# Optimization experiments

Hardware: AMD Instinct MI355X
Metric: run time of the kernel (lower is better)

## Reference

```python
import jax, jax.numpy as jnp
import numpy as np

DIM = 512
NUM_HEADS = 8
HEAD_DIM = DIM // NUM_HEADS
SOFT_CAP = 50.0
EPS = 1e-6
ROPE_BASE = 10000.0


def _rope_cos_sin(T):
    inv_freq = 1.0 / (ROPE_BASE ** (jnp.arange(0, HEAD_DIM, 2, dtype=jnp.float32) / HEAD_DIM))
    t = jnp.arange(T, dtype=jnp.float32)
    freqs = jnp.einsum('t,f->tf', t, inv_freq)            # (T, HEAD_DIM//2)
    emb = jnp.concatenate([freqs, freqs], axis=-1)         # (T, HEAD_DIM)
    return jnp.cos(emb), jnp.sin(emb)


def _rotate_half(x):
    x1, x2 = jnp.split(x, 2, axis=-1)
    return jnp.concatenate([-x2, x1], axis=-1)


def _apply_rope(x, cos, sin):
    # x: (B,H,T,hd); cos/sin: (T,hd) broadcast over B,H
    return x * cos + _rotate_half(x) * sin


def _rmsnorm(x, g):
    var = jnp.mean(jnp.square(x), axis=-1, keepdims=True)
    return x * jax.lax.rsqrt(var + EPS) * g


def setup_inputs() -> dict:
    key = jax.random.key(0)
    ks = jax.random.split(key, 7)
    B, T = 256, 256
    s = 1.0 / np.sqrt(DIM)
    return {
        'x': jax.random.normal(ks[0], (B, T, DIM), dtype=jnp.float32),
        'wq': jax.random.normal(ks[1], (DIM, DIM), dtype=jnp.float32) * s,
        'wk': jax.random.normal(ks[2], (DIM, DIM), dtype=jnp.float32) * s,
        'wv': jax.random.normal(ks[3], (DIM, DIM), dtype=jnp.float32) * s,
        'wo': jax.random.normal(ks[4], (DIM, DIM), dtype=jnp.float32) * s,
        'gq': jnp.ones((HEAD_DIM,), dtype=jnp.float32),
        'gk': jnp.ones((HEAD_DIM,), dtype=jnp.float32),
    }


def reference(x, wq, wk, wv, wo, gq, gk):
    B, T, D = x.shape
    H, hd = NUM_HEADS, HEAD_DIM
    scale = hd ** -0.5

    def proj(w):
        return jnp.einsum('btd,ed->bte', x, w).reshape(B, T, H, hd).transpose(0, 2, 1, 3)

    q = proj(wq)  # (B,H,T,hd)
    k = proj(wk)
    v = proj(wv)

    q = _rmsnorm(q, gq)
    k = _rmsnorm(k, gk)

    cos, sin = _rope_cos_sin(T)
    q = _apply_rope(q, cos, sin)
    k = _apply_rope(k, cos, sin)

    attn = jnp.einsum('bhqd,bhkd->bhqk', q, k) * scale
    attn = SOFT_CAP * jnp.tanh(attn / SOFT_CAP)
    causal = jnp.tril(jnp.ones((T, T), dtype=bool))
    attn = jnp.where(causal, attn, -jnp.inf)
    attn = jax.nn.softmax(attn.astype(jnp.float32), axis=-1).astype(v.dtype)

    out = jnp.einsum('bhqk,bhkd->bhqd', attn, v)
    out = out.transpose(0, 2, 1, 3).reshape(B, T, D)
    return jnp.einsum('btd,ed->bte', out, wo)
```

## Files before the change

### kernel.cpp

```cpp
#include <hip/hip_runtime.h>
#include <cstdint>
#include <cstddef>

#define B_   256
#define T_   256
#define D_   512
#define H_   8
#define HD_  64
#define BT_  65536
#define KDIM 512

typedef __bf16 bf16x8_t __attribute__((ext_vector_type(8)));
typedef __bf16 bf16x4_t __attribute__((ext_vector_type(4)));
typedef float  f32x4_t  __attribute__((ext_vector_type(4)));

__device__ __forceinline__ void gload16(const void* gp, void* lp) {
  __builtin_amdgcn_global_load_lds(
      (const __attribute__((address_space(1))) void*)gp,
      (__attribute__((address_space(3))) void*)lp, 16, 0, 0);
}

#define BAR()   __builtin_amdgcn_s_barrier()
#define SCB()   __builtin_amdgcn_sched_barrier(0)
#define LGKM0() asm volatile("s_waitcnt lgkmcnt(0)" ::: "memory")

__global__ __launch_bounds__(256) void prep(
    const float* __restrict__ x,
    const float* __restrict__ wq, const float* __restrict__ wk,
    const float* __restrict__ wv, const float* __restrict__ wo,
    __bf16* __restrict__ xb, __bf16* __restrict__ wb,
    float* __restrict__ rc, float* __restrict__ rs) {
  const int b = blockIdx.x;
  if (b < 2048) {
    for (size_t i = (size_t)b * 256 + threadIdx.x; i < 8388608UL; i += 524288UL) {
      f32x4_t v = *(const f32x4_t*)&x[i * 4];
      bf16x4_t o;
      o[0] = (__bf16)v[0]; o[1] = (__bf16)v[1]; o[2] = (__bf16)v[2]; o[3] = (__bf16)v[3];
      *(bf16x4_t*)&xb[i * 4] = o;
    }
  } else if (b < 2304) {
    for (int i = (b - 2048) * 256 + threadIdx.x; i < 262144; i += 65536) {
      int which = i >> 16;
      int off   = (i & 65535) * 4;
      const float* src = (which == 0) ? wq : (which == 1) ? wk : (which == 2) ? wv : wo;
      f32x4_t v = *(const f32x4_t*)&src[off];
      bf16x4_t o;
      o[0] = (__bf16)v[0]; o[1] = (__bf16)v[1]; o[2] = (__bf16)v[2]; o[3] = (__bf16)v[3];
      *(bf16x4_t*)&wb[(size_t)which * 262144 + off] = o;
    }
  } else {
    int idx = (b - 2304) * 256 + threadIdx.x;
    if (idx < T_ * 32) {
      int t = idx >> 5, j = idx & 31;
      float inv = powf(10000.f, -(float)j * (1.0f / 32.0f));
      float a = (float)t * inv;
      rc[idx] = cosf(a);
      rs[idx] = sinf(a);
    }
  }
}

template <int MODE>
__global__ __launch_bounds__(512, 2) void gemm256(
    const __bf16* __restrict__ A, const __bf16* __restrict__ W,
    void* __restrict__ outp) {
  __shared__ __bf16 lds[65536];
  const int tid = threadIdx.x;
  const int lane = tid & 63, w = tid >> 6;
  const int wm = w >> 2, wn = w & 3;
  const int l15 = lane & 15, lg = lane >> 4;
  const int swl = l15 & 7;

  const int cpx = gridDim.x >> 3;
  const int swz = (blockIdx.x & 7) * cpx + (blockIdx.x >> 3);
  const int bz = swz >> 9;
  const int by = (swz >> 1) & 255;
  const int bx = swz & 1;
  const int m0 = by * 256, n0 = bx * 256;

  const __bf16* Ag = A + (size_t)m0 * KDIM;
  const __bf16* Bg = W + (size_t)bz * (KDIM * KDIM) + (size_t)n0 * KDIM;
  const int srow = tid >> 3;
  const int scol = (((tid & 7) ^ ((tid >> 3) & 7)) * 8);

#define STAGE(J) do {                                                        \
    const int T__ = (J) >> 2, r__ = (J) & 3;                                 \
    const int h__ = r__ >> 1;                                                \
    const int isB__ = (r__ == 1 || r__ == 2);                                \
    const size_t grow__ = (size_t)(h__ * 128 + srow) * KDIM + T__ * 64 + scol; \
    const __bf16* gp__ = isB__ ? (Bg + grow__) : (Ag + grow__);              \
    __bf16* lp__ = &lds[(T__ & 1) * 32768 + isB__ * 16384 + (h__ * 128 + w * 8) * 64]; \
    gload16(gp__, lp__);                                                     \
    gload16(gp__ + 64 * KDIM, lp__ + 64 * 64);                               \
  } while (0)

  f32x4_t acc[8][4];
#pragma unroll
  for (int i = 0; i < 8; i++)
#pragma unroll
    for (int j = 0; j < 4; j++) acc[i][j] = (f32x4_t){0.f, 0.f, 0.f, 0.f};

  bf16x8_t a0[4][2], a1[4][2], b0[2][2], b1[2][2];

#define PH_A(P, STJ) do {                                                    \
    const int ab__ = (P) * 32768;                                            \
    _Pragma("unroll") for (int i = 0; i < 4; i++)                            \
      _Pragma("unroll") for (int s = 0; s < 2; s++)                          \
        a0[i][s] = *(const bf16x8_t*)&lds[ab__ + (wm * 64 + i * 16 + l15) * 64 + (((s * 4 + lg) ^ swl) << 3)]; \
    _Pragma("unroll") for (int j = 0; j < 2; j++)                            \
      _Pragma("unroll") for (int s = 0; s < 2; s++)                          \
        b0[j][s] = *(const bf16x8_t*)&lds[ab__ + 16384 + (wn * 32 + j * 16 + l15) * 64 + (((s * 4 + lg) ^ swl) << 3)]; \
    if ((STJ) >= 0) STAGE(STJ);                                              \
    SCB(); BAR(); LGKM0(); SCB();                                            \
    __builtin_amdgcn_s_setprio(1);                                           \
    _Pragma("unroll") for (int i = 0; i < 4; i++)                            \
      _Pragma("unroll") for (int j = 0; j < 2; j++) {                        \
        acc[i][j] = __builtin_amdgcn_mfma_f32_16x16x32_bf16(a0[i][0], b0[j][0], acc[i][j], 0, 0, 0); \
        acc[i][j] = __builtin_amdgcn_mfma_f32_16x16x32_bf16(a0[i][1], b0[j][1], acc[i][j], 0, 0, 0); \
      }                                                                      \
    __builtin_amdgcn_s_setprio(0); SCB(); BAR();                             \
  } while (0)

#define PH_B(P, STJ) do {                                                    \
    const int ab__ = (P) * 32768;                                            \
    _Pragma("unroll") for (int j = 0; j < 2; j++)                            \
      _Pragma("unroll") for (int s = 0; s < 2; s++)                          \
        b1[j][s] = *(const bf16x8_t*)&lds[ab__ + 16384 + (128 + wn * 32 + j * 16 + l15) * 64 + (((s * 4 + lg) ^ swl) << 3)]; \
    if ((STJ) >= 0) STAGE(STJ);                                              \
    SCB(); BAR(); LGKM0(); SCB();                                            \
    __builtin_amdgcn_s_setprio(1);                                           \
    _Pragma("unroll") for (int i = 0; i < 4; i++)                            \
      _Pragma("unroll") for (int j = 0; j < 2; j++) {                        \
        acc[i][j + 2] = __builtin_amdgcn_mfma_f32_16x16x32_bf16(a0[i][0], b1[j][0], acc[i][j + 2], 0, 0, 0); \
        acc[i][j + 2] = __builtin_amdgcn_mfma_f32_16x16x32_bf16(a0[i][1], b1[j][1], acc[i][j + 2], 0, 0, 0); \
      }                                                                      \
    __builtin_amdgcn_s_setprio(0); SCB(); BAR();                             \
  } while (0)

#define PH_C(P, STJ) do {                                                    \
    const int ab__ = (P) * 32768;                                            \
    _Pragma("unroll") for (int i = 0; i < 4; i++)                            \
      _Pragma("unroll") for (int s = 0; s < 2; s++)                          \
        a1[i][s] = *(const bf16x8_t*)&lds[ab__ + (128 + wm * 64 + i * 16 + l15) * 64 + (((s * 4 + lg) ^ swl) << 3)]; \
    if ((STJ) >= 0) STAGE(STJ);                                              \
    SCB(); BAR(); LGKM0(); SCB();                                            \
    __builtin_amdgcn_s_setprio(1);                                           \
    _Pragma("unroll") for (int i = 0; i < 4; i++)                            \
      _Pragma("unroll") for (int j = 0; j < 2; j++) {                        \
        acc[i + 4][j + 2] = __builtin_amdgcn_mfma_f32_16x16x32_bf16(a1[i][0], b1[j][0], acc[i + 4][j + 2], 0, 0, 0); \
        acc[i + 4][j + 2] = __builtin_amdgcn_mfma_f32_16x16x32_bf16(a1[i][1], b1[j][1], acc[i + 4][j + 2], 0, 0, 0); \
      }                                                                      \
    __builtin_amdgcn_s_setprio(0); SCB(); BAR();                             \
  } while (0)

#define PH_D(P, STJ, VM) do {                                                \
    if ((STJ) >= 0) STAGE(STJ);                                              \
    SCB(); BAR();                                                            \
    __builtin_amdgcn_s_setprio(1);                                           \
    _Pragma("unroll") for (int i = 0; i < 4; i++)                            \
      _Pragma("unroll") for (int j = 0; j < 2; j++) {                        \
        acc[i + 4][j] = __builtin_amdgcn_mfma_f32_16x16x32_bf16(a1[i][0], b0[j][0], acc[i + 4][j], 0, 0, 0); \
        acc[i + 4][j] = __builtin_amdgcn_mfma_f32_16x16x32_bf16(a1[i][1], b0[j][1], acc[i + 4][j], 0, 0, 0); \
      }                                                                      \
    __builtin_amdgcn_s_setprio(0);                                           \
    if ((VM) == 6) asm volatile("s_waitcnt vmcnt(6)" ::: "memory");          \
    else if ((VM) == 0) asm volatile("s_waitcnt vmcnt(0)" ::: "memory");     \
    SCB(); BAR();                                                            \
  } while (0)

  STAGE(0); STAGE(1); STAGE(2); STAGE(3); STAGE(4); STAGE(5); STAGE(6);
  asm volatile("s_waitcnt vmcnt(6)" ::: "memory");
  SCB(); BAR();

#pragma unroll 1
  for (int tp = 0; tp < 3; ++tp) {
    const int g0 = tp * 8;
    PH_A(0, g0 + 7);  PH_B(0, g0 + 8);  PH_C(0, g0 + 9);  PH_D(0, g0 + 10, 6);
    PH_A(1, g0 + 11); PH_B(1, g0 + 12); PH_C(1, g0 + 13); PH_D(1, g0 + 14, 6);
  }
  PH_A(0, 31); PH_B(0, -1); PH_C(0, -1); PH_D(0, -1, 0);
  PH_A(1, -1); PH_B(1, -1); PH_C(1, -1); PH_D(1, -1, -1);

#undef PH_A
#undef PH_B
#undef PH_C
#undef PH_D
#undef STAGE

#pragma unroll
  for (int i = 0; i < 8; i++) {
#pragma unroll
    for (int rr = 0; rr < 4; rr++) {
      const int m = m0 + (i >> 2) * 128 + wm * 64 + (i & 3) * 16 + lg * 4 + rr;
      if (MODE == 0) {
        __bf16* outz = (__bf16*)outp + (size_t)bz * ((size_t)BT_ * D_);
        const int bb = m >> 8, tt = m & 255;
        const size_t rbase = ((size_t)bb * H_) * T_ * HD_ + (size_t)tt * HD_;
#pragma unroll
        for (int j = 0; j < 4; j++) {
          const int c = n0 + (j >> 1) * 128 + wn * 32 + (j & 1) * 16 + l15;
          const int hh = c >> 6, dd = c & 63;
          outz[rbase + (size_t)hh * (T_ * HD_) + dd] = (__bf16)acc[i][j][rr];
        }
      } else {
        float* outf = (float*)outp;
#pragma unroll
        for (int j = 0; j < 4; j++) {
          const int c = n0 + (j >> 1) * 128 + wn * 32 + (j & 1) * 16 + l15;
          outf[(size_t)m * D_ + c] = acc[i][j][rr];
        }
      }
    }
  }
}

__global__ __launch_bounds__(256) void norm_rope(
    __bf16* __restrict__ qb, __bf16* __restrict__ kb,
    const float* __restrict__ gq, const float* __restrict__ gk,
    const float* __restrict__ rc, const float* __restrict__ rs) {
  const int gid = blockIdx.x * 256 + threadIdx.x;
  const int wid = gid >> 6;
  const int lane = gid & 63;
  const int l2 = lane & 31;
  const int half = lane >> 5;
  const int nw = (gridDim.x * 256) >> 6;
  const int NROWS = B_ * H_ * T_;
  for (int idx = wid; idx < NROWS; idx += nw) {
    int ri = idx * 2 + half;
    int isk = ri >= NROWS;
    int r = isk ? ri - NROWS : ri;
    __bf16* base = isk ? kb : qb;
    const float* g = isk ? gk : gq;
    size_t off = (size_t)r * HD_ + 2 * l2;
    unsigned u = *(const unsigned*)&base[off];
    float v0 = (float)__builtin_bit_cast(__bf16, (unsigned short)(u & 0xffffu));
    float v1 = (float)__builtin_bit_cast(__bf16, (unsigned short)(u >> 16));
    float ss = v0 * v0 + v1 * v1;
#pragma unroll
    for (int m = 1; m < 32; m <<= 1) ss += __shfl_xor(ss, m);
    float rn = rsqrtf(ss * (1.0f / HD_) + 1e-6f);
    v0 *= rn * g[2 * l2];
    v1 *= rn * g[2 * l2 + 1];
    int t = r & (T_ - 1);
    int j0 = (2 * l2) & 31;
    float c0 = rc[t * 32 + j0], c1 = rc[t * 32 + j0 + 1];
    float s0 = rs[t * 32 + j0], s1 = rs[t * 32 + j0 + 1];
    float p0 = __shfl_xor(v0, 16);
    float p1 = __shfl_xor(v1, 16);
    float sg = (l2 < 16) ? -1.f : 1.f;
    float o0 = v0 * c0 + sg * p0 * s0;
    float o1 = v1 * c1 + sg * p1 * s1;
    unsigned short h0 = __builtin_bit_cast(unsigned short, (__bf16)o0);
    unsigned short h1 = __builtin_bit_cast(unsigned short, (__bf16)o1);
    *(unsigned*)&base[off] = (unsigned)h0 | ((unsigned)h1 << 16);
  }
}

__global__ __launch_bounds__(512, 2) void attn_kernel(
    const __bf16* __restrict__ qb, const __bf16* __restrict__ kb,
    const __bf16* __restrict__ vb, __bf16* __restrict__ ob) {
  __shared__ __bf16 Kl[256 * 64];
  __shared__ __bf16 VT[64 * 256];
  __shared__ __bf16 Pl[8 * 16 * 64];
  const int bh = blockIdx.x;
  const __bf16* Qg = qb + (size_t)bh * (T_ * HD_);
  const __bf16* Kg = kb + (size_t)bh * (T_ * HD_);
  const __bf16* Vg = vb + (size_t)bh * (T_ * HD_);
  const int tid = threadIdx.x, lane = tid & 63, w = tid >> 6;
  const int bI = bh >> 3, hI = bh & 7;

#pragma unroll
  for (int p = 0; p < 4; p++) {
    const int t = p * 64 + (tid >> 3);
    const int a = tid & 7;
    const int d0 = a * 8;
    *(bf16x8_t*)&Kl[t * 64 + (((a ^ (t & 7)) << 3))] =
        *(const bf16x8_t*)&Kg[t * HD_ + d0];
    bf16x8_t vv = *(const bf16x8_t*)&Vg[t * HD_ + d0];
#pragma unroll
    for (int j = 0; j < 8; j++) {
      const int row = d0 + j;
      const int rk = (row & 7) ^ ((row >> 3) & 7);
      VT[row * 256 + (((t >> 3) ^ rk) << 3) + (t & 7)] = vv[j];
    }
  }
  __syncthreads();

  const int l15 = lane & 15;
  const int lg = lane >> 4;
  const int sw = l15 & 7;
  const f32x4_t zero = {0.f, 0.f, 0.f, 0.f};
  const float C1 = 0.0072134752f;
  const float LOG2E = 1.44269504f;

  for (int half = 0; half < 2; half++) {
    const int qt = half ? (15 - w) : w;
    const int q0 = qt * 16;
    bf16x8_t aq0 = *(const bf16x8_t*)&Qg[(q0 + l15) * HD_ + lg * 8];
    bf16x8_t aq1 = *(const bf16x8_t*)&Qg[(q0 + l15) * HD_ + 32 + lg * 8];
    const int ntiles_e = (qt + 2) & ~1;
    const int qr = q0 + (lg << 2);

    f32x4_t ls = {0.f, 0.f, 0.f, 0.f};
    f32x4_t o[4];
#pragma unroll
    for (int j = 0; j < 4; j++) o[j] = zero;

    for (int t0 = 0; t0 < ntiles_e; t0 += 4) {
      const int te = (t0 + 4 < ntiles_e) ? (t0 + 4) : ntiles_e;
      for (int n = t0; n < te; ++n) {
        bf16x8_t kb0 = *(const bf16x8_t*)&Kl[(n * 16 + l15) * 64 + ((lg ^ sw) << 3)];
        bf16x8_t kb1 = *(const bf16x8_t*)&Kl[(n * 16 + l15) * 64 + (((4 + lg) ^ sw) << 3)];
        f32x4_t a = __builtin_amdgcn_mfma_f32_16x16x32_bf16(aq0, kb0, zero, 0, 0, 0);
        a = __builtin_amdgcn_mfma_f32_16x16x32_bf16(aq1, kb1, a, 0, 0, 0);
        const int key = n * 16 + l15;
        const int lsl = ((n - t0) << 1) + (l15 >> 3);
#pragma unroll
        for (int r = 0; r < 4; r++) {
          float e2 = __builtin_amdgcn_exp2f(a[r] * C1);
          float cm = -100.f * __builtin_amdgcn_rcpf(e2 + 1.f);
          float p = __builtin_amdgcn_exp2f(cm * LOG2E);
          p = (key <= qr + r) ? p : 0.f;
          ls[r] += p;
          const int ro = (lg << 2) + r;
          Pl[w * 1024 + ro * 64 + ((lsl ^ (ro & 7)) << 3) + (l15 & 7)] = (__bf16)p;
        }
      }
      asm volatile("s_waitcnt lgkmcnt(0)" ::: "memory");
      __builtin_amdgcn_sched_barrier(0);
      const int nkc = (te - t0) >> 1;
      for (int kcc = 0; kcc < nkc; ++kcc) {
        bf16x8_t pa = *(const bf16x8_t*)&Pl[w * 1024 + l15 * 64 + (((kcc * 4 + lg) ^ sw) << 3)];
#pragma unroll
        for (int j = 0; j < 4; j++) {
          const int row = j * 16 + l15;
          const int rk = sw ^ ((2 * j + (l15 >> 3)) & 7);
          const int sl = (t0 << 1) + kcc * 4 + lg;
          bf16x8_t bv = *(const bf16x8_t*)&VT[row * 256 + ((sl ^ rk) << 3)];
          o[j] = __builtin_amdgcn_mfma_f32_16x16x32_bf16(pa, bv, o[j], 0, 0, 0);
        }
      }
    }

#pragma unroll
    for (int off = 1; off < 16; off <<= 1) {
#pragma unroll
      for (int r = 0; r < 4; r++) ls[r] += __shfl_xor(ls[r], off);
    }

    float rl[4];
#pragma unroll
    for (int r = 0; r < 4; r++) rl[r] = 1.0f / ls[r];
#pragma unroll
    for (int j = 0; j < 4; j++) {
      int dd = j * 16 + l15;
#pragma unroll
      for (int r = 0; r < 4; r++) {
        int q = qr + r;
        ob[((size_t)(bI * T_ + q)) * D_ + hI * HD_ + dd] = (__bf16)(o[j][r] * rl[r]);
      }
    }
  }
}

extern "C" void kernel_launch(void* const* d_in, const int* in_sizes, int n_in,
                              void* d_out, int out_size, void* d_ws, size_t ws_size,
                              hipStream_t stream) {
  (void)in_sizes; (void)n_in; (void)out_size; (void)ws_size;
  const float* x  = (const float*)d_in[0];
  const float* wq = (const float*)d_in[1];
  const float* wk = (const float*)d_in[2];
  const float* wv = (const float*)d_in[3];
  const float* wo = (const float*)d_in[4];
  const float* gq = (const float*)d_in[5];
  const float* gk = (const float*)d_in[6];

  char* ws = (char*)d_ws;
  __bf16* xb   = (__bf16*)ws;
  __bf16* qkvb = (__bf16*)(ws + 67108864UL);
  __bf16* qb = qkvb;
  __bf16* kb = qkvb + 33554432UL;
  __bf16* vb = qkvb + 67108864UL;
  __bf16* wb = (__bf16*)(ws + 4UL * 67108864UL);
  float*  rc = (float*)(ws + 4UL * 67108864UL + 2097152UL);
  float*  rs = rc + 8192;
  __bf16* ob = xb;

  prep<<<dim3(2336), 256, 0, stream>>>(x, wq, wk, wv, wo, xb, wb, rc, rs);
  gemm256<0><<<dim3(1536), 512, 0, stream>>>(xb, wb, (void*)qkvb);
  norm_rope<<<dim3(2048), 256, 0, stream>>>(qb, kb, gq, gk, rc, rs);
  attn_kernel<<<dim3(2048), 512, 0, stream>>>(qb, kb, vb, ob);
  gemm256<1><<<dim3(512), 512, 0, stream>>>(ob, wb + 3UL * 262144UL, d_out);
}
```

Before: 356.7 us.

## Make GEMM blocks loop over all N tiles for one M tile

Both GEMM launches now give each block one 256-row M tile and loop over every output N tile in turn (six jobs for QKV, two for the output projection). The load pipeline keeps prefetching across job boundaries, and each job is stored before the accumulators are cleared. The grid drops from 1536/512 blocks to 256. The aim is to remove per-block prologue and drain cost and keep the A tile hot in cache, at the cost of only one block per CU, which gives less latency hiding than the 2-per-CU launch bounds allow.

```diff
diff --git a/kernel.cpp b/kernel.cpp
--- a/kernel.cpp
+++ b/kernel.cpp
@@ -64,6 +64,7 @@
 __global__ __launch_bounds__(512, 2) void gemm256(
     const __bf16* __restrict__ A, const __bf16* __restrict__ W,
     void* __restrict__ outp) {
+  constexpr int NJOBS = (MODE == 0) ? 6 : 2;
   __shared__ __bf16 lds[65536];
   const int tid = threadIdx.x;
   const int lane = tid & 63, w = tid >> 6;
@@ -73,23 +74,23 @@
 
   const int cpx = gridDim.x >> 3;
   const int swz = (blockIdx.x & 7) * cpx + (blockIdx.x >> 3);
-  const int bz = swz >> 9;
-  const int by = (swz >> 1) & 255;
-  const int bx = swz & 1;
-  const int m0 = by * 256, n0 = bx * 256;
+  const int m0 = swz * 256;
 
   const __bf16* Ag = A + (size_t)m0 * KDIM;
-  const __bf16* Bg = W + (size_t)bz * (KDIM * KDIM) + (size_t)n0 * KDIM;
   const int srow = tid >> 3;
   const int scol = (((tid & 7) ^ ((tid >> 3) & 7)) * 8);
 
+#define BOFF(JB) ((MODE == 0) ? ((size_t)((JB) >> 1) * 262144 + (size_t)((JB) & 1) * 131072) \
+                              : ((size_t)(JB) * 131072))
+
 #define STAGE(J) do {                                                        \
-    const int T__ = (J) >> 2, r__ = (J) & 3;                                 \
+    const int jb__ = (J) >> 5;                                               \
+    const int Tl__ = ((J) >> 2) & 7, r__ = (J) & 3;                          \
     const int h__ = r__ >> 1;                                                \
     const int isB__ = (r__ == 1 || r__ == 2);                                \
-    const size_t grow__ = (size_t)(h__ * 128 + srow) * KDIM + T__ * 64 + scol; \
-    const __bf16* gp__ = isB__ ? (Bg + grow__) : (Ag + grow__);              \
-    __bf16* lp__ = &lds[(T__ & 1) * 32768 + isB__ * 16384 + (h__ * 128 + w * 8) * 64]; \
+    const size_t grow__ = (size_t)(h__ * 128 + srow) * KDIM + Tl__ * 64 + scol; \
+    const __bf16* gp__ = isB__ ? (W + BOFF(jb__) + grow__) : (Ag + grow__);  \
+    __bf16* lp__ = &lds[(((J) >> 2) & 1) * 32768 + isB__ * 16384 + (h__ * 128 + w * 8) * 64]; \
     gload16(gp__, lp__);                                                     \
     gload16(gp__ + 64 * KDIM, lp__ + 64 * 64);                               \
   } while (0)
@@ -173,45 +174,65 @@
   SCB(); BAR();
 
 #pragma unroll 1
-  for (int tp = 0; tp < 3; ++tp) {
-    const int g0 = tp * 8;
-    PH_A(0, g0 + 7);  PH_B(0, g0 + 8);  PH_C(0, g0 + 9);  PH_D(0, g0 + 10, 6);
-    PH_A(1, g0 + 11); PH_B(1, g0 + 12); PH_C(1, g0 + 13); PH_D(1, g0 + 14, 6);
+  for (int jb = 0; jb < NJOBS; ++jb) {
+    if (jb < NJOBS - 1) {
+#pragma unroll 1
+      for (int tp = 0; tp < 4; ++tp) {
+        const int g0 = jb * 32 + tp * 8;
+        PH_A(0, g0 + 7);  PH_B(0, g0 + 8);  PH_C(0, g0 + 9);  PH_D(0, g0 + 10, 6);
+        PH_A(1, g0 + 11); PH_B(1, g0 + 12); PH_C(1, g0 + 13); PH_D(1, g0 + 14, 6);
+      }
+    } else {
+#pragma unroll 1
+      for (int tp = 0; tp < 3; ++tp) {
+        const int g0 = jb * 32 + tp * 8;
+        PH_A(0, g0 + 7);  PH_B(0, g0 + 8);  PH_C(0, g0 + 9);  PH_D(0, g0 + 10, 6);
+        PH_A(1, g0 + 11); PH_B(1, g0 + 12); PH_C(1, g0 + 13); PH_D(1, g0 + 14, 6);
+      }
+      PH_A(0, jb * 32 + 31); PH_B(0, -1); PH_C(0, -1); PH_D(0, -1, 0);
+      PH_A(1, -1); PH_B(1, -1); PH_C(1, -1); PH_D(1, -1, -1);
+    }
+
+    {
+      const int n0j = (MODE == 0) ? ((jb & 1) * 256) : (jb * 256);
+#pragma unroll
+      for (int i = 0; i < 8; i++) {
+#pragma unroll
+        for (int rr = 0; rr < 4; rr++) {
+          const int m = m0 + (i >> 2) * 128 + wm * 64 + (i & 3) * 16 + lg * 4 + rr;
+          if (MODE == 0) {
+            __bf16* outz = (__bf16*)outp + (size_t)(jb >> 1) * ((size_t)BT_ * D_);
+            const int bb = m >> 8, tt = m & 255;
+            const size_t rbase = ((size_t)bb * H_) * T_ * HD_ + (size_t)tt * HD_;
+#pragma unroll
+            for (int j = 0; j < 4; j++) {
+              const int c = n0j + (j >> 1) * 128 + wn * 32 + (j & 1) * 16 + l15;
+              const int hh = c >> 6, dd = c & 63;
+              outz[rbase + (size_t)hh * (T_ * HD_) + dd] = (__bf16)acc[i][j][rr];
+            }
+          } else {
+            float* outf = (float*)outp;
+#pragma unroll
+            for (int j = 0; j < 4; j++) {
+              const int c = n0j + (j >> 1) * 128 + wn * 32 + (j & 1) * 16 + l15;
+              outf[(size_t)m * D_ + c] = acc[i][j][rr];
+            }
+          }
+        }
+      }
+#pragma unroll
+      for (int i = 0; i < 8; i++)
+#pragma unroll
+        for (int j = 0; j < 4; j++) acc[i][j] = (f32x4_t){0.f, 0.f, 0.f, 0.f};
+    }
   }
-  PH_A(0, 31); PH_B(0, -1); PH_C(0, -1); PH_D(0, -1, 0);
-  PH_A(1, -1); PH_B(1, -1); PH_C(1, -1); PH_D(1, -1, -1);
 
 #undef PH_A
 #undef PH_B
 #undef PH_C
 #undef PH_D
 #undef STAGE
-
-#pragma unroll
-  for (int i = 0; i < 8; i++) {
-#pragma unroll
-    for (int rr = 0; rr < 4; rr++) {
-      const int m = m0 + (i >> 2) * 128 + wm * 64 + (i & 3) * 16 + lg * 4 + rr;
-      if (MODE == 0) {
-        __bf16* outz = (__bf16*)outp + (size_t)bz * ((size_t)BT_ * D_);
-        const int bb = m >> 8, tt = m & 255;
-        const size_t rbase = ((size_t)bb * H_) * T_ * HD_ + (size_t)tt * HD_;
-#pragma unroll
-        for (int j = 0; j < 4; j++) {
-          const int c = n0 + (j >> 1) * 128 + wn * 32 + (j & 1) * 16 + l15;
-          const int hh = c >> 6, dd = c & 63;
-          outz[rbase + (size_t)hh * (T_ * HD_) + dd] = (__bf16)acc[i][j][rr];
-        }
-      } else {
-        float* outf = (float*)outp;
-#pragma unroll
-        for (int j = 0; j < 4; j++) {
-          const int c = n0 + (j >> 1) * 128 + wn * 32 + (j & 1) * 16 + l15;
-          outf[(size_t)m * D_ + c] = acc[i][j][rr];
-        }
-      }
-    }
-  }
+#undef BOFF
 }
 
 __global__ __launch_bounds__(256) void norm_rope(
@@ -387,8 +408,8 @@
   __bf16* ob = xb;
 
   prep<<<dim3(2336), 256, 0, stream>>>(x, wq, wk, wv, wo, xb, wb, rc, rs);
-  gemm256<0><<<dim3(1536), 512, 0, stream>>>(xb, wb, (void*)qkvb);
+  gemm256<0><<<dim3(256), 512, 0, stream>>>(xb, wb, (void*)qkvb);
   norm_rope<<<dim3(2048), 256, 0, stream>>>(qb, kb, gq, gk, rc, rs);
   attn_kernel<<<dim3(2048), 512, 0, stream>>>(qb, kb, vb, ob);
-  gemm256<1><<<dim3(512), 512, 0, stream>>>(ob, wb + 3UL * 262144UL, d_out);
-}
+  gemm256<1><<<dim3(256), 512, 0, stream>>>(ob, wb + 3UL * 262144UL, d_out);
+}
```

Result: slower. 423.9 us (+18.8%).

## Fuse QK RMSNorm and RoPE into attention kernel, remap QKV GEMM tile order

Applied to the files above, without the earlier changes.

Removes the separate norm_rope pass. Q and K RMSNorm plus rotary embedding are now applied in registers while Q and K are loaded inside the attention kernel, which drops a full read and write of the Q and K buffers. The QKV GEMM block index mapping also changes so that the three projections for one row tile sit next to each other, which should improve reuse of the A tile in L2. In exchange, the attention kernel does extra work in its prologue and needs more registers.

```diff
diff --git a/kernel.cpp b/kernel.cpp
--- a/kernel.cpp
+++ b/kernel.cpp
@@ -73,10 +73,18 @@
 
   const int cpx = gridDim.x >> 3;
   const int swz = (blockIdx.x & 7) * cpx + (blockIdx.x >> 3);
-  const int bz = swz >> 9;
-  const int by = (swz >> 1) & 255;
-  const int bx = swz & 1;
-  const int m0 = by * 256, n0 = bx * 256;
+  int m_idx, bz, bx;
+  if (MODE == 0) {
+    m_idx = swz / 6;
+    const int rem = swz - m_idx * 6;
+    bz = rem >> 1;
+    bx = rem & 1;
+  } else {
+    m_idx = swz >> 1;
+    bz = 0;
+    bx = swz & 1;
+  }
+  const int m0 = m_idx * 256, n0 = bx * 256;
 
   const __bf16* Ag = A + (size_t)m0 * KDIM;
   const __bf16* Bg = W + (size_t)bz * (KDIM * KDIM) + (size_t)n0 * KDIM;
@@ -214,51 +222,11 @@
   }
 }
 
-__global__ __launch_bounds__(256) void norm_rope(
-    __bf16* __restrict__ qb, __bf16* __restrict__ kb,
+__global__ __launch_bounds__(512, 2) void attn_kernel(
+    const __bf16* __restrict__ qb, const __bf16* __restrict__ kb,
+    const __bf16* __restrict__ vb, __bf16* __restrict__ ob,
     const float* __restrict__ gq, const float* __restrict__ gk,
     const float* __restrict__ rc, const float* __restrict__ rs) {
-  const int gid = blockIdx.x * 256 + threadIdx.x;
-  const int wid = gid >> 6;
-  const int lane = gid & 63;
-  const int l2 = lane & 31;
-  const int half = lane >> 5;
-  const int nw = (gridDim.x * 256) >> 6;
-  const int NROWS = B_ * H_ * T_;
-  for (int idx = wid; idx < NROWS; idx += nw) {
-    int ri = idx * 2 + half;
-    int isk = ri >= NROWS;
-    int r = isk ? ri - NROWS : ri;
-    __bf16* base = isk ? kb : qb;
-    const float* g = isk ? gk : gq;
-    size_t off = (size_t)r * HD_ + 2 * l2;
-    unsigned u = *(const unsigned*)&base[off];
-    float v0 = (float)__builtin_bit_cast(__bf16, (unsigned short)(u & 0xffffu));
-    float v1 = (float)__builtin_bit_cast(__bf16, (unsigned short)(u >> 16));
-    float ss = v0 * v0 + v1 * v1;
-#pragma unroll
-    for (int m = 1; m < 32; m <<= 1) ss += __shfl_xor(ss, m);
-    float rn = rsqrtf(ss * (1.0f / HD_) + 1e-6f);
-    v0 *= rn * g[2 * l2];
-    v1 *= rn * g[2 * l2 + 1];
-    int t = r & (T_ - 1);
-    int j0 = (2 * l2) & 31;
-    float c0 = rc[t * 32 + j0], c1 = rc[t * 32 + j0 + 1];
-    float s0 = rs[t * 32 + j0], s1 = rs[t * 32 + j0 + 1];
-    float p0 = __shfl_xor(v0, 16);
-    float p1 = __shfl_xor(v1, 16);
-    float sg = (l2 < 16) ? -1.f : 1.f;
-    float o0 = v0 * c0 + sg * p0 * s0;
-    float o1 = v1 * c1 + sg * p1 * s1;
-    unsigned short h0 = __builtin_bit_cast(unsigned short, (__bf16)o0);
-    unsigned short h1 = __builtin_bit_cast(unsigned short, (__bf16)o1);
-    *(unsigned*)&base[off] = (unsigned)h0 | ((unsigned)h1 << 16);
-  }
-}
-
-__global__ __launch_bounds__(512, 2) void attn_kernel(
-    const __bf16* __restrict__ qb, const __bf16* __restrict__ kb,
-    const __bf16* __restrict__ vb, __bf16* __restrict__ ob) {
   __shared__ __bf16 Kl[256 * 64];
   __shared__ __bf16 VT[64 * 256];
   __shared__ __bf16 Pl[8 * 16 * 64];
@@ -274,8 +242,34 @@
     const int t = p * 64 + (tid >> 3);
     const int a = tid & 7;
     const int d0 = a * 8;
-    *(bf16x8_t*)&Kl[t * 64 + (((a ^ (t & 7)) << 3))] =
-        *(const bf16x8_t*)&Kg[t * HD_ + d0];
+    bf16x8_t kv = *(const bf16x8_t*)&Kg[t * HD_ + d0];
+    float kf[8], ss = 0.f;
+#pragma unroll
+    for (int j = 0; j < 8; j++) { kf[j] = (float)kv[j]; ss += kf[j] * kf[j]; }
+    ss += __shfl_xor(ss, 1); ss += __shfl_xor(ss, 2); ss += __shfl_xor(ss, 4);
+    const float rn = rsqrtf(ss * 0.015625f + 1e-6f);
+    const f32x4_t gk0 = *(const f32x4_t*)&gk[d0];
+    const f32x4_t gk1 = *(const f32x4_t*)&gk[d0 + 4];
+    float vn[8];
+#pragma unroll
+    for (int j = 0; j < 8; j++) vn[j] = kf[j] * rn * ((j < 4) ? gk0[j] : gk1[j - 4]);
+    float pn[8];
+#pragma unroll
+    for (int j = 0; j < 8; j++) pn[j] = __shfl_xor(vn[j], 4);
+    const int f0 = (a & 3) * 8;
+    const f32x4_t c0 = *(const f32x4_t*)&rc[t * 32 + f0];
+    const f32x4_t c1 = *(const f32x4_t*)&rc[t * 32 + f0 + 4];
+    const f32x4_t s0 = *(const f32x4_t*)&rs[t * 32 + f0];
+    const f32x4_t s1 = *(const f32x4_t*)&rs[t * 32 + f0 + 4];
+    const float sg = (a < 4) ? -1.f : 1.f;
+    bf16x8_t ko;
+#pragma unroll
+    for (int j = 0; j < 8; j++) {
+      const float cc = (j < 4) ? c0[j] : c1[j - 4];
+      const float sS = (j < 4) ? s0[j] : s1[j - 4];
+      ko[j] = (__bf16)(vn[j] * cc + sg * pn[j] * sS);
+    }
+    *(bf16x8_t*)&Kl[t * 64 + (((a ^ (t & 7)) << 3))] = ko;
     bf16x8_t vv = *(const bf16x8_t*)&Vg[t * HD_ + d0];
 #pragma unroll
     for (int j = 0; j < 8; j++) {
@@ -296,8 +290,38 @@
   for (int half = 0; half < 2; half++) {
     const int qt = half ? (15 - w) : w;
     const int q0 = qt * 16;
-    bf16x8_t aq0 = *(const bf16x8_t*)&Qg[(q0 + l15) * HD_ + lg * 8];
-    bf16x8_t aq1 = *(const bf16x8_t*)&Qg[(q0 + l15) * HD_ + 32 + lg * 8];
+    const int tq = q0 + l15;
+    bf16x8_t q0r = *(const bf16x8_t*)&Qg[tq * HD_ + lg * 8];
+    bf16x8_t q1r = *(const bf16x8_t*)&Qg[tq * HD_ + 32 + lg * 8];
+    float qf0[8], qf1[8], qss = 0.f;
+#pragma unroll
+    for (int j = 0; j < 8; j++) {
+      qf0[j] = (float)q0r[j]; qf1[j] = (float)q1r[j];
+      qss += qf0[j] * qf0[j] + qf1[j] * qf1[j];
+    }
+    qss += __shfl_xor(qss, 16); qss += __shfl_xor(qss, 32);
+    const float qrn = rsqrtf(qss * 0.015625f + 1e-6f);
+    const f32x4_t gqa = *(const f32x4_t*)&gq[lg * 8];
+    const f32x4_t gqb2 = *(const f32x4_t*)&gq[lg * 8 + 4];
+    const f32x4_t gqc = *(const f32x4_t*)&gq[32 + lg * 8];
+    const f32x4_t gqd = *(const f32x4_t*)&gq[32 + lg * 8 + 4];
+    const f32x4_t qc0 = *(const f32x4_t*)&rc[tq * 32 + lg * 8];
+    const f32x4_t qc1 = *(const f32x4_t*)&rc[tq * 32 + lg * 8 + 4];
+    const f32x4_t qs0 = *(const f32x4_t*)&rs[tq * 32 + lg * 8];
+    const f32x4_t qs1 = *(const f32x4_t*)&rs[tq * 32 + lg * 8 + 4];
+    bf16x8_t aq0, aq1;
+#pragma unroll
+    for (int j = 0; j < 8; j++) {
+      const float glo = (j < 4) ? gqa[j] : gqb2[j - 4];
+      const float ghi = (j < 4) ? gqc[j] : gqd[j - 4];
+      const float cc  = (j < 4) ? qc0[j] : qc1[j - 4];
+      const float sS  = (j < 4) ? qs0[j] : qs1[j - 4];
+      const float vlo = qf0[j] * qrn * glo;
+      const float vhi = qf1[j] * qrn * ghi;
+      aq0[j] = (__bf16)(vlo * cc - vhi * sS);
+      aq1[j] = (__bf16)(vhi * cc + vlo * sS);
+    }
+
     const int ntiles_e = (qt + 2) & ~1;
     const int qr = q0 + (lg << 2);
 
@@ -388,7 +412,6 @@
 
   prep<<<dim3(2336), 256, 0, stream>>>(x, wq, wk, wv, wo, xb, wb, rc, rs);
   gemm256<0><<<dim3(1536), 512, 0, stream>>>(xb, wb, (void*)qkvb);
-  norm_rope<<<dim3(2048), 256, 0, stream>>>(qb, kb, gq, gk, rc, rs);
-  attn_kernel<<<dim3(2048), 512, 0, stream>>>(qb, kb, vb, ob);
+  attn_kernel<<<dim3(2048), 512, 0, stream>>>(qb, kb, vb, ob, gq, gk, rc, rs);
   gemm256<1><<<dim3(512), 512, 0, stream>>>(ob, wb + 3UL * 262144UL, d_out);
 }
```

Measured after the change: 303.8 us. 1.17x faster.
